# Optimization experiments

Hardware: AMD Instinct MI355X
Metric: run time of the kernel (lower is better)

Reference implementation:

```python
import jax, jax.numpy as jnp
import numpy as np

EMB = 768
HEADS = 12
HEAD_DIM = EMB // HEADS
FF = 4 * EMB
EPS = 1e-5


def setup_inputs() -> dict:
    key = jax.random.key(0)
    ks = jax.random.split(key, 12)
    s = 0.02
    return {
        "x": jax.random.normal(ks[0], (4, 2048, EMB), dtype=jnp.float32),
        "ln1_scale": jnp.ones((EMB,), jnp.float32),
        "ln1_shift": jnp.zeros((EMB,), jnp.float32),
        # weights stored [in, out] (transpose of torch Linear layout)
        "wq": jax.random.normal(ks[1], (EMB, EMB), jnp.float32) * s,
        "wk": jax.random.normal(ks[2], (EMB, EMB), jnp.float32) * s,
        "wv": jax.random.normal(ks[3], (EMB, EMB), jnp.float32) * s,
        "wo": jax.random.normal(ks[4], (EMB, EMB), jnp.float32) * s,
        "bo": jnp.zeros((EMB,), jnp.float32),
        "ln2_scale": jnp.ones((EMB,), jnp.float32),
        "ln2_shift": jnp.zeros((EMB,), jnp.float32),
        "w1": jax.random.normal(ks[5], (EMB, FF), jnp.float32) * s,
        "b1": jnp.zeros((FF,), jnp.float32),
        "w2": jax.random.normal(ks[6], (FF, EMB), jnp.float32) * s,
        "b2": jnp.zeros((EMB,), jnp.float32),
    }


def _layernorm(x, scale, shift):
    mean = jnp.mean(x, axis=-1, keepdims=True)
    var = jnp.mean(jnp.square(x - mean), axis=-1, keepdims=True)  # unbiased=False
    return scale * (x - mean) / jnp.sqrt(var + EPS) + shift


def _gelu_tanh(x):
    c = jnp.sqrt(jnp.float32(2.0 / np.pi))
    return 0.5 * x * (1.0 + jnp.tanh(c * (x + 0.044715 * x * x * x)))


def _attention(x, wq, wk, wv, wo, bo):
    b, s, _ = x.shape
    q = (x @ wq).reshape(b, s, HEADS, HEAD_DIM).transpose(0, 2, 1, 3)
    k = (x @ wk).reshape(b, s, HEADS, HEAD_DIM).transpose(0, 2, 1, 3)
    v = (x @ wv).reshape(b, s, HEADS, HEAD_DIM).transpose(0, 2, 1, 3)
    scores = jnp.einsum("bhqd,bhkd->bhqk", q, k)  # [B,H,S,S]
    causal = jnp.tril(jnp.ones((s, s), dtype=bool))
    scores = jnp.where(causal, scores, -jnp.inf)
    weights = jax.nn.softmax(scores / jnp.sqrt(jnp.float32(HEAD_DIM)), axis=-1)
    ctx = jnp.einsum("bhqk,bhkd->bhqd", weights, v)
    ctx = ctx.transpose(0, 2, 1, 3).reshape(b, s, EMB)
    return ctx @ wo + bo


def reference(x, ln1_scale, ln1_shift, wq, wk, wv, wo, bo,
              ln2_scale, ln2_shift, w1, b1, w2, b2):
    # dropout rate is 0.0 (inference) -> identity
    x = x + _attention(_layernorm(x, ln1_scale, ln1_shift), wq, wk, wv, wo, bo)
    h = _layernorm(x, ln2_scale, ln2_shift)
    h = _gelu_tanh(h @ w1 + b1) @ w2 + b2
    return x + h
```

## Files before the change

kernel.cpp:

```cpp
#include <hip/hip_runtime.h>
#include <stdint.h>

#define EMB 768
#define SEQ 2048
#define BATCH 4
#define NHEADS 12
#define HDIM 64
#define FFDIM 3072
#define NTOK (BATCH*SEQ)
#define LNEPS 1e-5f
#define QSCALE 0.1803368801111137f

typedef __attribute__((ext_vector_type(8))) short bf16x8;
typedef __attribute__((ext_vector_type(4))) float f32x4;
typedef __attribute__((ext_vector_type(16))) float f32x16;

__device__ __forceinline__ uint16_t f2bf(float f){
  union { float f; uint32_t u; } v; v.f = f;
  uint32_t r = v.u + 0x7fffu + ((v.u >> 16) & 1u);
  return (uint16_t)(r >> 16);
}
__device__ __forceinline__ uint32_t cvt_pk_bf16(float lo, float hi){
  uint32_t d;
  asm("v_cvt_pk_bf16_f32 %0, %1, %2" : "=v"(d) : "v"(lo), "v"(hi));
  return d;
}

typedef __attribute__((address_space(3))) uint32_t lds32_t;
typedef __attribute__((address_space(1))) const uint32_t glb32_t;
__device__ __forceinline__ void gload16(const void* g, void* l){
  __builtin_amdgcn_global_load_lds((glb32_t*)(uintptr_t)g,
                                   (lds32_t*)(uintptr_t)l, 16, 0, 0);
}

struct TPtrs { const float* src[6]; uint16_t* dst[6]; };
__global__ __launch_bounds__(256) void transpose_all(TPtrs tp){
  int idx = blockIdx.x;
  int which, bx, by, K, N;
  if (idx < 2304){ which = idx/576; int l = idx - which*576; bx = l%24; by = l/24; K = 768;  N = 768;  }
  else if (idx < 4608){ which = 4; int l = idx-2304; bx = l%96; by = l/96; K = 768;  N = 3072; }
  else { which = 5; int l = idx-4608; bx = l%24; by = l/24; K = 3072; N = 768;  }
  const float* w = tp.src[which];
  uint16_t* wt   = tp.dst[which];
  __shared__ uint16_t tile[32][33];
  int n0 = bx*32, k0 = by*32;
  #pragma unroll
  for (int i=0;i<4;i++){
    int k = threadIdx.y + i*8;
    tile[k][threadIdx.x] = f2bf(w[(size_t)(k0+k)*N + n0 + threadIdx.x]);
  }
  __syncthreads();
  #pragma unroll
  for (int i=0;i<4;i++){
    int n = threadIdx.y + i*8;
    wt[(size_t)(n0+n)*K + k0 + threadIdx.x] = tile[threadIdx.x][n];
  }
}

__global__ __launch_bounds__(256) void ln_kernel(const float* __restrict__ x,
    const float* __restrict__ sc, const float* __restrict__ sh,
    uint16_t* __restrict__ out)
{
  int row = blockIdx.x*4 + (threadIdx.x>>6);
  int ln = threadIdx.x & 63;
  const float4* xr = (const float4*)(x + (size_t)row*EMB);
  float4 v0 = xr[ln], v1 = xr[64+ln], v2 = xr[128+ln];
  float s  = v0.x+v0.y+v0.z+v0.w + v1.x+v1.y+v1.z+v1.w + v2.x+v2.y+v2.z+v2.w;
  float s2 = v0.x*v0.x+v0.y*v0.y+v0.z*v0.z+v0.w*v0.w
           + v1.x*v1.x+v1.y*v1.y+v1.z*v1.z+v1.w*v1.w
           + v2.x*v2.x+v2.y*v2.y+v2.z*v2.z+v2.w*v2.w;
  #pragma unroll
  for (int off=1;off<64;off<<=1){ s += __shfl_xor(s,off); s2 += __shfl_xor(s2,off); }
  float mean = s*(1.f/768.f);
  float var  = s2*(1.f/768.f) - mean*mean;
  float rstd = rsqrtf(var + LNEPS);
  uint16_t* orow = out + (size_t)row*EMB;
  float4 vv[3] = {v0,v1,v2};
  #pragma unroll
  for (int i=0;i<3;i++){
    int c = (i*64+ln)*4;
    ushort4 o4;
    o4.x = f2bf((vv[i].x-mean)*rstd*sc[c+0] + sh[c+0]);
    o4.y = f2bf((vv[i].y-mean)*rstd*sc[c+1] + sh[c+1]);
    o4.z = f2bf((vv[i].z-mean)*rstd*sc[c+2] + sh[c+2]);
    o4.w = f2bf((vv[i].w-mean)*rstd*sc[c+3] + sh[c+3]);
    *(ushort4*)(orow + c) = o4;
  }
}

template<int MODE, int TM>
__global__ __launch_bounds__(256, 4) void gemm_bt(const uint16_t* __restrict__ A,
    const uint16_t* __restrict__ Bt0,
    const float* __restrict__ bias,
    const float* __restrict__ resid,
    void* __restrict__ outp,
    uint16_t* __restrict__ vt_out,
    int N, int K, long bt_zstride, long out_zstride)
{
  constexpr int MI = TM/32;
  __shared__ __align__(16) uint16_t As[2][TM][32];
  __shared__ __align__(16) uint16_t Bs[2][128][32];
  const uint16_t* Bt = Bt0 + (size_t)blockIdx.z * bt_zstride;
  int tid = threadIdx.x;
  int wave = tid>>6, ln = tid&63, lane16 = ln&15, quad = ln>>4;
  int m0 = blockIdx.x*TM, n0 = blockIdx.y*128;
  int wm = (wave>>1)*(MI*16), wn = (wave&1)*64;
  f32x4 zf = {0.f,0.f,0.f,0.f};
  f32x4 acc[MI][4];
  #pragma unroll
  for (int i=0;i<MI;i++)
    #pragma unroll
    for (int j=0;j<4;j++) acc[i][j]=zf;
  int ar = tid>>2;
  int ac = (tid&3)*8;
  const uint16_t* Arow0 = A  + (size_t)(m0+ar)*K    + ac;
  const uint16_t* Arow1 = A  + (size_t)(m0+ar+64)*K + ac;
  const uint16_t* Brow0 = Bt + (size_t)(n0+ar)*K    + ac;
  const uint16_t* Brow1 = Bt + (size_t)(n0+ar+64)*K + ac;

  auto stage = [&](int buf, int k0){
    char* lA = (char*)&As[buf][0][0] + wave*1024;
    char* lB = (char*)&Bs[buf][0][0] + wave*1024;
    gload16(Arow0 + k0, lA);
    if (TM==128) gload16(Arow1 + k0, lA + 4096);
    gload16(Brow0 + k0, lB);
    gload16(Brow1 + k0, lB + 4096);
  };

  int niter = K>>5;
  stage(0, 0);
  for (int s=0; s<niter; s++){
    __syncthreads();
    if (s+1 < niter) stage((s+1)&1, (s+1)<<5);
    int buf = s&1;
    bf16x8 af[MI], bfr[4];
    #pragma unroll
    for (int mi=0;mi<MI;mi++) af[mi]  = *(const bf16x8*)&As[buf][wm+mi*16+lane16][quad*8];
    #pragma unroll
    for (int ni=0;ni<4;ni++)  bfr[ni] = *(const bf16x8*)&Bs[buf][wn+ni*16+lane16][quad*8];
    #pragma unroll
    for (int mi=0;mi<MI;mi++)
      #pragma unroll
      for (int ni=0;ni<4;ni++)
        acc[mi][ni] = __builtin_amdgcn_mfma_f32_16x16x32_bf16(af[mi], bfr[ni], acc[mi][ni], 0,0,0);
  }
  if (MODE==0 && blockIdx.z==2){
    #pragma unroll
    for (int mi=0;mi<MI;mi++){
      int mrow0 = m0 + wm + mi*16 + quad*4;
      int bb = mrow0 >> 11, s = mrow0 & 2047;
      #pragma unroll
      for (int ni=0;ni<4;ni++){
        int ncol = n0 + wn + ni*16 + lane16;
        int hh = ncol >> 6, dd = ncol & 63;
        ushort4 o4 = { f2bf(acc[mi][ni][0]), f2bf(acc[mi][ni][1]),
                       f2bf(acc[mi][ni][2]), f2bf(acc[mi][ni][3]) };
        *(ushort4*)(vt_out + ((size_t)((bb*NHEADS+hh)*HDIM + dd))*SEQ + s) = o4;
      }
    }
    return;
  }
  float oscale = (MODE==0 && blockIdx.z==0) ? QSCALE : 1.0f;
  #pragma unroll
  for (int mi=0;mi<MI;mi++){
    #pragma unroll
    for (int r=0;r<4;r++){
      int mrow = m0 + wm + mi*16 + quad*4 + r;
      #pragma unroll
      for (int ni=0;ni<4;ni++){
        int ncol = n0 + wn + ni*16 + lane16;
        float vv = acc[mi][ni][r];
        size_t idx = (size_t)mrow*N + ncol;
        if (MODE==0){
          ((uint16_t*)outp)[(size_t)blockIdx.z*out_zstride + idx] = f2bf(vv*oscale);
        } else if (MODE==1){
          ((float*)outp)[idx] = vv + bias[ncol] + resid[idx];
        } else if (MODE==2){
          float t = vv + bias[ncol];
          float u = 1.5957691216057308f*(t + 0.044715f*t*t*t);
          ((uint16_t*)outp)[idx] = f2bf(t / (1.f + __expf(-u)));
        } else {
          ((float*)outp)[idx] = vv + bias[ncol] + resid[idx];
        }
      }
    }
  }
}

__global__ __launch_bounds__(128, 2) void attn_kernel(const uint16_t* __restrict__ q,
    const uint16_t* __restrict__ k, const uint16_t* __restrict__ vt,
    uint16_t* __restrict__ ctx)
{
  __shared__ __align__(16) uint16_t Ks[2][8][64][8];
  __shared__ __align__(16) uint16_t Vs[2][8][64][8];
  int tid = threadIdx.x;
  int wave = tid>>6, ln = tid&63, l32 = ln&31, h5 = ln>>5;
  int id  = blockIdx.x;
  int xcd = id & 7;
  int s_  = id >> 3;
  int p   = s_ & 15;
  int g   = xcd*6 + (s_ >> 4);
  int h   = g % NHEADS, b = g / NHEADS;
  size_t kgbase = ((size_t)(b*SEQ + ln))*EMB + h*HDIM;
  size_t vgbase = ((size_t)((b*NHEADS + h)*HDIM + ln))*SEQ;

  f32x16 o0, o1;
  float m_l, l_l;
  bf16x8 qb[4];
  int q0w, myq;

  auto stage = [&](int buf, int kv0){
    #pragma unroll
    for (int i=0;i<4;i++){
      int c = wave + 2*i;
      gload16(k  + kgbase + (size_t)kv0*EMB + c*8, &Ks[buf][c][0][0]);
      gload16(vt + vgbase + kv0 + c*8,             &Vs[buf][c][0][0]);
    }
  };
  auto init_tile = [&](int tile){
    q0w = tile*64 + wave*32;
    myq = q0w + l32;
    const uint16_t* qrow = q + ((size_t)(b*SEQ + myq))*EMB + h*HDIM + h5*8;
    #pragma unroll
    for (int dm=0;dm<4;dm++) qb[dm] = *(const bf16x8*)(qrow + dm*16);
    #pragma unroll
    for (int r=0;r<16;r++){ o0[r]=0.f; o1[r]=0.f; }
    m_l = -3.0e38f; l_l = 0.f;
  };
  auto writeout = [&](){
    float inv = 1.0f / l_l;
    uint16_t* crow = ctx + ((size_t)(b*SEQ + myq))*EMB + h*HDIM + 4*h5;
    #pragma unroll
    for (int rr=0; rr<4; rr++){
      ushort4 w0 = { f2bf(o0[4*rr+0]*inv), f2bf(o0[4*rr+1]*inv),
                     f2bf(o0[4*rr+2]*inv), f2bf(o0[4*rr+3]*inv) };
      *(ushort4*)(crow + rr*8) = w0;
      ushort4 w1 = { f2bf(o1[4*rr+0]*inv), f2bf(o1[4*rr+1]*inv),
                     f2bf(o1[4*rr+2]*inv), f2bf(o1[4*rr+3]*inv) };
      *(ushort4*)(crow + 32 + rr*8) = w1;
    }
  };
  auto compute = [&](int buf, int kv0, bool masked){
    f32x16 st0, st1;
    #pragma unroll
    for (int r=0;r<16;r++){ st0[r]=0.f; st1[r]=0.f; }
    __builtin_amdgcn_s_setprio(1);
    #pragma unroll
    for (int dm=0;dm<4;dm++){
      bf16x8 ka0 = *(const bf16x8*)&Ks[buf][dm*2+h5][l32][0];
      bf16x8 ka1 = *(const bf16x8*)&Ks[buf][dm*2+h5][32+l32][0];
      st0 = __builtin_amdgcn_mfma_f32_32x32x16_bf16(ka0, qb[dm], st0, 0,0,0);
      st1 = __builtin_amdgcn_mfma_f32_32x32x16_bf16(ka1, qb[dm], st1, 0,0,0);
    }
    __builtin_amdgcn_s_setprio(0);
    if (masked){
      #pragma unroll
      for (int r=0;r<16;r++){
        int kvr = kv0 + (r&3) + 8*(r>>2) + 4*h5;
        if (kvr      > myq) st0[r] = -1e30f;
        if (kvr + 32 > myq) st1[r] = -1e30f;
      }
    }
    bf16x8 va[4][2];
    #pragma unroll
    for (int ks=0;ks<4;ks++){
      va[ks][0] = *(const bf16x8*)&Vs[buf][ks*2+h5][l32][0];
      va[ks][1] = *(const bf16x8*)&Vs[buf][ks*2+h5][32+l32][0];
    }
    float t[8];
    #pragma unroll
    for (int r=0;r<8;r++)
      t[r] = fmaxf(fmaxf(st0[r], st0[r+8]), fmaxf(st1[r], st1[r+8]));
    t[0]=fmaxf(t[0],t[4]); t[1]=fmaxf(t[1],t[5]);
    t[2]=fmaxf(t[2],t[6]); t[3]=fmaxf(t[3],t[7]);
    float cm = fmaxf(fmaxf(t[0],t[1]), fmaxf(t[2],t[3]));
    cm = fmaxf(cm, __shfl_xor(cm, 32));
    if (!__all(cm - m_l <= 6.0f)){
      float mn = fmaxf(m_l, cm);
      float alpha = __builtin_amdgcn_exp2f(m_l - mn);
      l_l *= alpha;
      #pragma unroll
      for (int r=0;r<16;r++){ o0[r]*=alpha; o1[r]*=alpha; }
      m_l = mn;
    }
    #pragma unroll
    for (int r=0;r<16;r++){
      st0[r] = __builtin_amdgcn_exp2f(st0[r] - m_l);
      st1[r] = __builtin_amdgcn_exp2f(st1[r] - m_l);
    }
    float s0=0.f, s1=0.f, s2=0.f, s3=0.f;
    #pragma unroll
    for (int r=0;r<16;r+=4){
      s0 += st0[r+0] + st1[r+0];
      s1 += st0[r+1] + st1[r+1];
      s2 += st0[r+2] + st1[r+2];
      s3 += st0[r+3] + st1[r+3];
    }
    float rs = (s0+s1)+(s2+s3);
    rs += __shfl_xor(rs, 32);
    l_l += rs;
    bf16x8 pbv[4];
    #pragma unroll
    for (int ks=0;ks<4;ks++){
      const int bs = (ks&1)*8;
      uint32_t c0,c1,c2,c3;
      if (ks < 2){
        c0 = cvt_pk_bf16(st0[bs+0], st0[bs+1]);
        c1 = cvt_pk_bf16(st0[bs+2], st0[bs+3]);
        c2 = cvt_pk_bf16(st0[bs+4], st0[bs+5]);
        c3 = cvt_pk_bf16(st0[bs+6], st0[bs+7]);
      } else {
        c0 = cvt_pk_bf16(st1[bs+0], st1[bs+1]);
        c1 = cvt_pk_bf16(st1[bs+2], st1[bs+3]);
        c2 = cvt_pk_bf16(st1[bs+4], st1[bs+5]);
        c3 = cvt_pk_bf16(st1[bs+6], st1[bs+7]);
      }
      uint32_t ya = (uint32_t)__shfl_xor((int)(h5 ? c0 : c2), 32);
      uint32_t yb = (uint32_t)__shfl_xor((int)(h5 ? c1 : c3), 32);
      union { uint32_t u[4]; bf16x8 v; } pu;
      pu.u[0] = h5 ? ya : c0;
      pu.u[1] = h5 ? yb : c1;
      pu.u[2] = h5 ? c2 : ya;
      pu.u[3] = h5 ? c3 : yb;
      pbv[ks] = pu.v;
    }
    __builtin_amdgcn_s_setprio(1);
    #pragma unroll
    for (int ks=0;ks<4;ks++){
      o0 = __builtin_amdgcn_mfma_f32_32x32x16_bf16(va[ks][0], pbv[ks], o0, 0,0,0);
      o1 = __builtin_amdgcn_mfma_f32_32x32x16_bf16(va[ks][1], pbv[ks], o1, 0,0,0);
    }
    __builtin_amdgcn_s_setprio(0);
  };

  int n0 = p + 1, ntot = 33;
  init_tile(p);
  stage(0, 0);
  for (int s=0; s<ntot; s++){
    int sl = (s < n0) ? s : s - n0;
    int kv0 = sl*64;
    __syncthreads();
    if (s+1 < ntot){
      int sn = s+1;
      int snl = (sn < n0) ? sn : sn - n0;
      stage(sn&1, snl*64);
    }
    if (s == n0){ writeout(); init_tile(31 - p); }
    bool masked = (s == n0-1) || (s == ntot-1);
    compute(s&1, kv0, masked);
  }
  writeout();
}

extern "C" void kernel_launch(void* const* d_in, const int* in_sizes, int n_in,
                              void* d_out, int out_size, void* d_ws, size_t ws_size,
                              hipStream_t stream) {
  const float* x     = (const float*)d_in[0];
  const float* ln1_s = (const float*)d_in[1];
  const float* ln1_b = (const float*)d_in[2];
  const float* wq    = (const float*)d_in[3];
  const float* wk    = (const float*)d_in[4];
  const float* wv    = (const float*)d_in[5];
  const float* wo    = (const float*)d_in[6];
  const float* bo    = (const float*)d_in[7];
  const float* ln2_s = (const float*)d_in[8];
  const float* ln2_b = (const float*)d_in[9];
  const float* w1    = (const float*)d_in[10];
  const float* b1    = (const float*)d_in[11];
  const float* w2    = (const float*)d_in[12];
  const float* b2    = (const float*)d_in[13];

  uint16_t* wqkv_t = (uint16_t*)d_ws;
  uint16_t* wo_t   = wqkv_t + 3*EMB*EMB;
  uint16_t* w1_t   = wo_t   + EMB*EMB;
  uint16_t* w2_t   = w1_t   + (size_t)FFDIM*EMB;
  uint16_t* xn     = w2_t   + (size_t)EMB*FFDIM;
  uint16_t* qkv    = xn     + (size_t)NTOK*EMB;
  uint16_t* ctx    = qkv    + (size_t)3*NTOK*EMB;
  uint16_t* hff    = qkv;
  float*    x1     = (float*)(ctx + (size_t)NTOK*EMB);
  uint16_t* vt     = (uint16_t*)(x1 + (size_t)NTOK*EMB);

  TPtrs tp;
  tp.src[0]=wq; tp.src[1]=wk; tp.src[2]=wv; tp.src[3]=wo; tp.src[4]=w1; tp.src[5]=w2;
  tp.dst[0]=wqkv_t; tp.dst[1]=wqkv_t+EMB*EMB; tp.dst[2]=wqkv_t+2*EMB*EMB;
  tp.dst[3]=wo_t; tp.dst[4]=w1_t; tp.dst[5]=w2_t;
  transpose_all<<<6912, dim3(32,8), 0, stream>>>(tp);

  ln_kernel<<<NTOK/4, 256, 0, stream>>>(x, ln1_s, ln1_b, xn);
  gemm_bt<0,128><<<dim3(NTOK/128, EMB/128, 3), 256, 0, stream>>>(
      xn, wqkv_t, nullptr, nullptr, qkv, vt, EMB, EMB,
      (long)EMB*EMB, (long)NTOK*EMB);
  attn_kernel<<<768, 128, 0, stream>>>(
      qkv, qkv + (size_t)NTOK*EMB, vt, ctx);
  gemm_bt<1,64><<<dim3(NTOK/64, EMB/128, 1), 256, 0, stream>>>(
      ctx, wo_t, bo, x, x1, nullptr, EMB, EMB, 0, 0);
  ln_kernel<<<NTOK/4, 256, 0, stream>>>(x1, ln2_s, ln2_b, xn);
  gemm_bt<2,128><<<dim3(NTOK/128, FFDIM/128, 1), 256, 0, stream>>>(
      xn, w1_t, b1, nullptr, hff, nullptr, FFDIM, EMB, 0, 0);
  gemm_bt<3,64><<<dim3(NTOK/64, EMB/128, 1), 256, 0, stream>>>(
      hff, w2_t, b2, x1, d_out, nullptr, EMB, FFDIM, 0, 0);
}
```

Baseline: 391.4 us.

## Split attention KV range across two waves per 32-query slice with LDS merge

```diff
diff --git a/kernel.cpp b/kernel.cpp
--- a/kernel.cpp
+++ b/kernel.cpp
@@ -187,70 +187,51 @@
   }
 }
 
-__global__ __launch_bounds__(128, 2) void attn_kernel(const uint16_t* __restrict__ q,
+__global__ __launch_bounds__(128, 3) void attn_kernel(const uint16_t* __restrict__ q,
     const uint16_t* __restrict__ k, const uint16_t* __restrict__ vt,
     uint16_t* __restrict__ ctx)
 {
-  __shared__ __align__(16) uint16_t Ks[2][8][64][8];
-  __shared__ __align__(16) uint16_t Vs[2][8][64][8];
+  __shared__ float cmb[64][35];
   int tid = threadIdx.x;
-  int wave = tid>>6, ln = tid&63, l32 = ln&31, h5 = ln>>5;
+  int wv = tid>>6, ln = tid&63, l32 = ln&31, h5 = ln>>5;
   int id  = blockIdx.x;
   int xcd = id & 7;
   int s_  = id >> 3;
-  int p   = s_ & 15;
-  int g   = xcd*6 + (s_ >> 4);
+  int sp  = s_ & 31;
+  int g   = xcd*6 + (s_ >> 5);
   int h   = g % NHEADS, b = g / NHEADS;
-  size_t kgbase = ((size_t)(b*SEQ + ln))*EMB + h*HDIM;
-  size_t vgbase = ((size_t)((b*NHEADS + h)*HDIM + ln))*SEQ;
+
+  const uint16_t* krow = k  + ((size_t)(b*SEQ) + l32)*EMB + h*HDIM + h5*8;
+  const uint16_t* vrow = vt + ((size_t)((b*NHEADS + h)*HDIM + l32))*SEQ + h5*8;
 
   f32x16 o0, o1;
   float m_l, l_l;
   bf16x8 qb[4];
-  int q0w, myq;
-
-  auto stage = [&](int buf, int kv0){
-    #pragma unroll
-    for (int i=0;i<4;i++){
-      int c = wave + 2*i;
-      gload16(k  + kgbase + (size_t)kv0*EMB + c*8, &Ks[buf][c][0][0]);
-      gload16(vt + vgbase + kv0 + c*8,             &Vs[buf][c][0][0]);
-    }
-  };
-  auto init_tile = [&](int tile){
-    q0w = tile*64 + wave*32;
-    myq = q0w + l32;
-    const uint16_t* qrow = q + ((size_t)(b*SEQ + myq))*EMB + h*HDIM + h5*8;
-    #pragma unroll
-    for (int dm=0;dm<4;dm++) qb[dm] = *(const bf16x8*)(qrow + dm*16);
-    #pragma unroll
-    for (int r=0;r<16;r++){ o0[r]=0.f; o1[r]=0.f; }
-    m_l = -3.0e38f; l_l = 0.f;
-  };
-  auto writeout = [&](){
-    float inv = 1.0f / l_l;
-    uint16_t* crow = ctx + ((size_t)(b*SEQ + myq))*EMB + h*HDIM + 4*h5;
-    #pragma unroll
-    for (int rr=0; rr<4; rr++){
-      ushort4 w0 = { f2bf(o0[4*rr+0]*inv), f2bf(o0[4*rr+1]*inv),
-                     f2bf(o0[4*rr+2]*inv), f2bf(o0[4*rr+3]*inv) };
-      *(ushort4*)(crow + rr*8) = w0;
-      ushort4 w1 = { f2bf(o1[4*rr+0]*inv), f2bf(o1[4*rr+1]*inv),
-                     f2bf(o1[4*rr+2]*inv), f2bf(o1[4*rr+3]*inv) };
-      *(ushort4*)(crow + 32 + rr*8) = w1;
-    }
-  };
-  auto compute = [&](int buf, int kv0, bool masked){
+  int myq;
+
+  auto compute = [&](int kv0, bool masked){
+    const uint16_t* kA = krow + (size_t)kv0*EMB;
+    const uint16_t* vA = vrow + kv0;
+    bf16x8 va[4][2];
+    #pragma unroll
+    for (int ks=0;ks<4;ks++){
+      va[ks][0] = *(const bf16x8*)(vA + ks*16);
+      va[ks][1] = *(const bf16x8*)(vA + 32*SEQ + ks*16);
+    }
+    bf16x8 kf0[4], kf1[4];
+    #pragma unroll
+    for (int dm=0;dm<4;dm++){
+      kf0[dm] = *(const bf16x8*)(kA + dm*16);
+      kf1[dm] = *(const bf16x8*)(kA + (size_t)32*EMB + dm*16);
+    }
     f32x16 st0, st1;
     #pragma unroll
     for (int r=0;r<16;r++){ st0[r]=0.f; st1[r]=0.f; }
     __builtin_amdgcn_s_setprio(1);
     #pragma unroll
     for (int dm=0;dm<4;dm++){
-      bf16x8 ka0 = *(const bf16x8*)&Ks[buf][dm*2+h5][l32][0];
-      bf16x8 ka1 = *(const bf16x8*)&Ks[buf][dm*2+h5][32+l32][0];
-      st0 = __builtin_amdgcn_mfma_f32_32x32x16_bf16(ka0, qb[dm], st0, 0,0,0);
-      st1 = __builtin_amdgcn_mfma_f32_32x32x16_bf16(ka1, qb[dm], st1, 0,0,0);
+      st0 = __builtin_amdgcn_mfma_f32_32x32x16_bf16(kf0[dm], qb[dm], st0, 0,0,0);
+      st1 = __builtin_amdgcn_mfma_f32_32x32x16_bf16(kf1[dm], qb[dm], st1, 0,0,0);
     }
     __builtin_amdgcn_s_setprio(0);
     if (masked){
@@ -260,12 +241,6 @@
         if (kvr      > myq) st0[r] = -1e30f;
         if (kvr + 32 > myq) st1[r] = -1e30f;
       }
-    }
-    bf16x8 va[4][2];
-    #pragma unroll
-    for (int ks=0;ks<4;ks++){
-      va[ks][0] = *(const bf16x8*)&Vs[buf][ks*2+h5][l32][0];
-      va[ks][1] = *(const bf16x8*)&Vs[buf][ks*2+h5][32+l32][0];
     }
     float t[8];
     #pragma unroll
@@ -333,23 +308,51 @@
     __builtin_amdgcn_s_setprio(0);
   };
 
-  int n0 = p + 1, ntot = 33;
-  init_tile(p);
-  stage(0, 0);
-  for (int s=0; s<ntot; s++){
-    int sl = (s < n0) ? s : s - n0;
-    int kv0 = sl*64;
+  auto do_slice = [&](int sl, int si){
+    myq = sl*32 + l32;
+    const uint16_t* qrow = q + ((size_t)(b*SEQ + myq))*EMB + h*HDIM + h5*8;
+    #pragma unroll
+    for (int dm=0;dm<4;dm++) qb[dm] = *(const bf16x8*)(qrow + dm*16);
+    #pragma unroll
+    for (int r=0;r<16;r++){ o0[r]=0.f; o1[r]=0.f; }
+    m_l = -3.0e38f; l_l = 0.f;
+    int tdiag = sl >> 1;
+    for (int t = (wv ^ si) & 1; t <= tdiag; t += 2)
+      compute(t*64, t == tdiag);
+    if (wv == 1){
+      cmb[ln][0] = m_l; cmb[ln][1] = l_l;
+      #pragma unroll
+      for (int r=0;r<16;r++){ cmb[ln][2+r] = o0[r]; cmb[ln][18+r] = o1[r]; }
+    }
     __syncthreads();
-    if (s+1 < ntot){
-      int sn = s+1;
-      int snl = (sn < n0) ? sn : sn - n0;
-      stage(sn&1, snl*64);
-    }
-    if (s == n0){ writeout(); init_tile(31 - p); }
-    bool masked = (s == n0-1) || (s == ntot-1);
-    compute(s&1, kv0, masked);
-  }
-  writeout();
+    if (wv == 0){
+      float m1 = cmb[ln][0], l1 = cmb[ln][1];
+      float mn = fmaxf(m_l, m1);
+      float a0 = __builtin_amdgcn_exp2f(m_l - mn);
+      float a1 = __builtin_amdgcn_exp2f(m1 - mn);
+      float inv = 1.0f / (l_l*a0 + l1*a1);
+      uint16_t* crow = ctx + ((size_t)(b*SEQ + myq))*EMB + h*HDIM + 4*h5;
+      #pragma unroll
+      for (int rr=0; rr<4; rr++){
+        ushort4 w0 = {
+          f2bf((o0[4*rr+0]*a0 + cmb[ln][2+4*rr+0]*a1)*inv),
+          f2bf((o0[4*rr+1]*a0 + cmb[ln][2+4*rr+1]*a1)*inv),
+          f2bf((o0[4*rr+2]*a0 + cmb[ln][2+4*rr+2]*a1)*inv),
+          f2bf((o0[4*rr+3]*a0 + cmb[ln][2+4*rr+3]*a1)*inv) };
+        *(ushort4*)(crow + rr*8) = w0;
+        ushort4 w1 = {
+          f2bf((o1[4*rr+0]*a0 + cmb[ln][18+4*rr+0]*a1)*inv),
+          f2bf((o1[4*rr+1]*a0 + cmb[ln][18+4*rr+1]*a1)*inv),
+          f2bf((o1[4*rr+2]*a0 + cmb[ln][18+4*rr+2]*a1)*inv),
+          f2bf((o1[4*rr+3]*a0 + cmb[ln][18+4*rr+3]*a1)*inv) };
+        *(ushort4*)(crow + 32 + rr*8) = w1;
+      }
+    }
+    __syncthreads();
+  };
+
+  do_slice(sp, 0);
+  do_slice(63 - sp, 1);
 }
 
 extern "C" void kernel_launch(void* const* d_in, const int* in_sizes, int n_in,
@@ -391,7 +394,7 @@
   gemm_bt<0,128><<<dim3(NTOK/128, EMB/128, 3), 256, 0, stream>>>(
       xn, wqkv_t, nullptr, nullptr, qkv, vt, EMB, EMB,
       (long)EMB*EMB, (long)NTOK*EMB);
-  attn_kernel<<<768, 128, 0, stream>>>(
+  attn_kernel<<<1536, 128, 0, stream>>>(
       qkv, qkv + (size_t)NTOK*EMB, vt, ctx);
   gemm_bt<1,64><<<dim3(NTOK/64, EMB/128, 1), 256, 0, stream>>>(
       ctx, wo_t, bo, x, x1, nullptr, EMB, EMB, 0, 0);
```

New measurement: 407.9 us. 4.2% more time.
